# Optimization experiments

Hardware: AMD Instinct MI355X
Metric: run time of the kernel (lower is better)

Reference implementation:

```python
import jax, jax.numpy as jnp
import numpy as np

B, N, L, K, C1 = 128, 300, 600, 19, 100  # batch, num_cnns, input_length, filter_size, fc hidden
PS = 7  # pool size == stride
LC = L - (K - 1)               # 582, conv output length
LP = (LC - PS) // PS + 1       # 83, pooled length
NC = 2                         # num_classes
EPS = 1e-5


def _bn(x, g, b, m, v):
    # eval-mode batchnorm, params broadcast along given axes already
    return g * (x - m) * jax.lax.rsqrt(v + EPS) + b


def setup_inputs() -> dict:
    key = jax.random.key(0)
    ks = jax.random.split(key, 20)
    f = lambda i, shape, s=0.1: (jax.random.normal(ks[i], shape, dtype=jnp.float32) * s)
    pv = lambda i, shape: (jax.random.uniform(ks[i], shape, dtype=jnp.float32) + 0.5)
    return {
        'x': jax.random.normal(ks[0], (B, 4, L), dtype=jnp.float32),
        'conv_w': f(1, (N, 4, K)), 'conv_b': f(2, (N,)),
        'bn1_g': pv(3, (N,)), 'bn1_b': f(4, (N,)), 'bn1_m': f(5, (N,)), 'bn1_v': pv(6, (N,)),
        'fc1_w': f(7, (N, C1, LP)), 'fc1_b': f(8, (N, C1)),
        'bn2_g': pv(9, (N, C1)), 'bn2_b': f(10, (N, C1)), 'bn2_m': f(11, (N, C1)), 'bn2_v': pv(12, (N, C1)),
        'fc2_w': f(13, (N, C1)), 'fc2_b': f(14, (N,)),
        'bn3_g': pv(15, (N,)), 'bn3_b': f(16, (N,)), 'bn3_m': f(17, (N,)), 'bn3_v': pv(18, (N,)),
        'final_w': f(19, (NC, N)), 'final_b': jnp.zeros((NC,), dtype=jnp.float32),
    }


def reference(x, conv_w, conv_b, bn1_g, bn1_b, bn1_m, bn1_v,
              fc1_w, fc1_b, bn2_g, bn2_b, bn2_m, bn2_v,
              fc2_w, fc2_b, bn3_g, bn3_b, bn3_m, bn3_v,
              final_w, final_b):
    # grouped conv on a repeated input == plain conv with 4 in-channels, N out-channels
    h = jax.lax.conv_general_dilated(x, conv_w, window_strides=(1,), padding='VALID',
                                     dimension_numbers=('NCH', 'OIH', 'NCH'))  # [B,N,582]
    h = h + conv_b[None, :, None]
    h = _bn(h, bn1_g[None, :, None], bn1_b[None, :, None], bn1_m[None, :, None], bn1_v[None, :, None])
    h = jnp.exp(h)
    # MaxPool1d(7,7): [B,N,582] -> [B,N,83]
    h = jax.lax.reduce_window(h, -jnp.inf, jax.lax.max,
                              window_dimensions=(1, 1, PS), window_strides=(1, 1, PS), padding='VALID')
    # grouped 1x1 conv == per-unit dense: [B,N,83] x [N,100,83] -> [B,N,100]
    h = jnp.einsum('bnp,nhp->bnh', h, fc1_w) + fc1_b[None]
    h = jax.nn.relu(_bn(h, bn2_g[None], bn2_b[None], bn2_m[None], bn2_v[None]))
    # second grouped 1x1 conv: [B,N,100] x [N,100] -> [B,N]
    h = jnp.einsum('bnh,nh->bn', h, fc2_w) + fc2_b[None]
    h = jax.nn.relu(_bn(h, bn3_g[None], bn3_b[None], bn3_m[None], bn3_v[None]))
    return h @ final_w.T + final_b  # [B,num_classes]
```

## Files before the change

kernel.cpp:

```cpp
#include <hip/hip_runtime.h>
#include <math.h>

#define EPS_ 1e-5f

__global__ __launch_bounds__(256) void kP(const float* __restrict__ fc1w,
                                          const float* __restrict__ conv_w,
                                          float* __restrict__ w1T,
                                          float* __restrict__ cwT) {
    __shared__ float sm[22800];
    const int blk = blockIdx.x, tid = threadIdx.x;
    if (blk < 300) {
        for (int i = tid; i < 8300; i += 256) {
            const int h = i / 83, p = i - h * 83;
            sm[p * 101 + h] = fc1w[(size_t)blk * 8300 + i];
        }
        __syncthreads();
        for (int i = tid; i < 8300; i += 256) {
            const int p = i / 100, h = i - p * 100;
            w1T[(size_t)blk * 8300 + i] = sm[p * 101 + h];
        }
    } else {
        for (int i = tid; i < 22800; i += 256) sm[i] = conv_w[i];
        __syncthreads();
        for (int i = tid; i < 22800; i += 256) {
            const int k = i / 300, n = i - k * 300;
            cwT[i] = sm[n * 76 + k];
        }
    }
}

__global__ __launch_bounds__(64) void kA(
        const float* __restrict__ x,
        const float* __restrict__ cwT,
        const float* __restrict__ conv_b,
        const float* __restrict__ g1, const float* __restrict__ b1,
        const float* __restrict__ m1, const float* __restrict__ v1,
        float* __restrict__ pooled)
{
    const int id  = blockIdx.x;
    const int b   = id / 112;
    const int sub = id - b * 112;
    if (sub >= 105) return;
    const int ng  = sub / 21;
    const int pc  = sub - ng * 21;
    const int p0c = pc * 4;
    const int p0  = (p0c > 79) ? 79 : p0c;
    const int lane = threadIdx.x;
    const int n   = ng * 64 + lane;
    const int nc  = (n < 300) ? n : 299;

    float acc[28];
    #pragma unroll
    for (int i = 0; i < 28; ++i) acc[i] = 0.f;

    #pragma unroll 1
    for (int c = 0; c < 4; ++c) {
        const float* xc = x + b * 2400 + c * 600 + 7 * p0;
        float xw[46];
        #pragma unroll
        for (int j = 0; j < 46; ++j) xw[j] = xc[j];
        const float* wc = cwT + c * 19 * 300 + nc;
        #pragma unroll
        for (int k = 0; k < 19; ++k) {
            const float wv = wc[k * 300];
            #pragma unroll
            for (int p = 0; p < 4; ++p)
                #pragma unroll
                for (int q = 0; q < 7; ++q)
                    acc[p * 7 + q] = fmaf(xw[7 * p + q + k], wv, acc[p * 7 + q]);
        }
    }

    const float A1 = g1[nc] * rsqrtf(v1[nc] + EPS_);
    const float B1 = fmaf(A1, conv_b[nc] - m1[nc], b1[nc]);
    if (n < 300) {
        float* op = pooled + ((size_t)n * 83 + p0) * 128 + b;
        #pragma unroll
        for (int p = 0; p < 4; ++p) {
            float mx = -INFINITY;
            #pragma unroll
            for (int q = 0; q < 7; ++q)
                mx = fmaxf(mx, fmaf(A1, acc[p * 7 + q], B1));
            op[p * 128] = __expf(mx);
        }
    }
}

__global__ __launch_bounds__(128) void kB(
        const float* __restrict__ pooled,
        const float* __restrict__ w1T,
        const float* __restrict__ fc1b,
        const float* __restrict__ g2, const float* __restrict__ b2,
        const float* __restrict__ m2, const float* __restrict__ v2,
        const float* __restrict__ fc2w,
        const float* __restrict__ fc2b,
        const float* __restrict__ g3, const float* __restrict__ b3,
        const float* __restrict__ m3, const float* __restrict__ v3,
        float* __restrict__ sout)
{
    __shared__ float sRed[2][64];
    const int id = blockIdx.x;
    const int bh = id / 304;
    const int n  = id - bh * 304;
    if (n >= 300) return;
    const int tid  = threadIdx.x;
    const int lane = tid & 63;
    const int hh   = __builtin_amdgcn_readfirstlane(tid >> 6);
    const int h0   = hh * 50;
    const int bb   = bh * 64 + lane;

    const float* pp = pooled + (size_t)n * 83 * 128 + bb;
    const float* wp = w1T + (size_t)n * 8300 + h0;

    float acc[50];
    #pragma unroll
    for (int j = 0; j < 50; ++j) acc[j] = 0.f;

    #pragma unroll 2
    for (int p = 0; p < 83; ++p) {
        const float pv = pp[p * 128];
        #pragma unroll
        for (int j = 0; j < 50; ++j)
            acc[j] = fmaf(pv, wp[p * 100 + j], acc[j]);
    }

    const int base = n * 100 + h0;
    float part = 0.f;
    #pragma unroll
    for (int j = 0; j < 50; ++j) {
        const float A2 = g2[base + j] * rsqrtf(v2[base + j] + EPS_);
        const float C2 = fmaf(A2, fc1b[base + j] - m2[base + j], b2[base + j]);
        const float act = fmaxf(fmaf(A2, acc[j], C2), 0.f);
        part = fmaf(act, fc2w[base + j], part);
    }
    sRed[hh][lane] = part;
    __syncthreads();
    if (tid < 64) {
        float s = sRed[0][tid] + sRed[1][tid] + fc2b[n];
        const float A3 = g3[n] * rsqrtf(v3[n] + EPS_);
        const float z = fmaf(A3, s - m3[n], b3[n]);
        sout[n * 128 + bh * 64 + tid] = fmaxf(z, 0.f);
    }
}

__global__ __launch_bounds__(64) void kC(
        const float* __restrict__ sout,
        const float* __restrict__ fw,
        const float* __restrict__ fb,
        float* __restrict__ out)
{
    const int b = blockIdx.x, t = threadIdx.x;
    float a0 = 0.f, a1 = 0.f;
    for (int nn = t; nn < 300; nn += 64) {
        const float v = sout[nn * 128 + b];
        a0 = fmaf(v, fw[nn], a0);
        a1 = fmaf(v, fw[300 + nn], a1);
    }
    #pragma unroll
    for (int off = 32; off > 0; off >>= 1) {
        a0 += __shfl_xor(a0, off, 64);
        a1 += __shfl_xor(a1, off, 64);
    }
    if (t == 0) {
        out[b * 2 + 0] = a0 + fb[0];
        out[b * 2 + 1] = a1 + fb[1];
    }
}

extern "C" void kernel_launch(void* const* d_in, const int* in_sizes, int n_in,
                              void* d_out, int out_size, void* d_ws, size_t ws_size,
                              hipStream_t stream) {
    const float* x      = (const float*)d_in[0];
    const float* conv_w = (const float*)d_in[1];
    const float* conv_b = (const float*)d_in[2];
    const float* g1 = (const float*)d_in[3];
    const float* b1 = (const float*)d_in[4];
    const float* m1 = (const float*)d_in[5];
    const float* v1 = (const float*)d_in[6];
    const float* fc1_w = (const float*)d_in[7];
    const float* fc1_b = (const float*)d_in[8];
    const float* g2 = (const float*)d_in[9];
    const float* b2 = (const float*)d_in[10];
    const float* m2 = (const float*)d_in[11];
    const float* v2 = (const float*)d_in[12];
    const float* fc2_w = (const float*)d_in[13];
    const float* fc2_b = (const float*)d_in[14];
    const float* g3 = (const float*)d_in[15];
    const float* b3 = (const float*)d_in[16];
    const float* m3 = (const float*)d_in[17];
    const float* v3 = (const float*)d_in[18];
    const float* fw = (const float*)d_in[19];
    const float* fb = (const float*)d_in[20];
    float* out = (float*)d_out;

    float* pooled = (float*)d_ws;
    float* w1T    = pooled + (size_t)300 * 83 * 128;
    float* cwT    = w1T + (size_t)300 * 8300;
    float* sout   = cwT + 22800;

    kP<<<301, 256, 0, stream>>>(fc1_w, conv_w, w1T, cwT);
    kA<<<128 * 112, 64, 0, stream>>>(x, cwT, conv_b, g1, b1, m1, v1, pooled);
    kB<<<608, 128, 0, stream>>>(pooled, w1T, fc1_b, g2, b2, m2, v2,
                                fc2_w, fc2_b, g3, b3, m3, v3, sout);
    kC<<<128, 64, 0, stream>>>(sout, fw, fb, out);
}
```

Baseline: 189.8 us.

## Widen blocks across prep, conv and FC kernels to raise occupancy

The prep kernel no longer allocates a 91 KB shared array. Its conv-weight transpose is spread over 76 small blocks instead of one, which cuts LDS use and raises occupancy for the fc1 transpose blocks. The conv kernel packs four 64-lane work items into 256-thread blocks, giving fewer, larger blocks. The FC kernel splits the 100 hidden units over four waves (28/28/28/16) instead of two, which lowers register pressure per thread and adds parallelism. In exchange there is an uneven last wave and an extra shared-memory reduction step.

```diff
diff --git a/kernel.cpp b/kernel.cpp
--- a/kernel.cpp
+++ b/kernel.cpp
@@ -7,9 +7,9 @@
                                           const float* __restrict__ conv_w,
                                           float* __restrict__ w1T,
                                           float* __restrict__ cwT) {
-    __shared__ float sm[22800];
     const int blk = blockIdx.x, tid = threadIdx.x;
     if (blk < 300) {
+        __shared__ float sm[83 * 101];
         for (int i = tid; i < 8300; i += 256) {
             const int h = i / 83, p = i - h * 83;
             sm[p * 101 + h] = fc1w[(size_t)blk * 8300 + i];
@@ -20,16 +20,13 @@
             w1T[(size_t)blk * 8300 + i] = sm[p * 101 + h];
         }
     } else {
-        for (int i = tid; i < 22800; i += 256) sm[i] = conv_w[i];
-        __syncthreads();
-        for (int i = tid; i < 22800; i += 256) {
-            const int k = i / 300, n = i - k * 300;
-            cwT[i] = sm[n * 76 + k];
-        }
-    }
-}
-
-__global__ __launch_bounds__(64) void kA(
+        const int k = blk - 300;
+        for (int n = tid; n < 300; n += 256)
+            cwT[k * 300 + n] = conv_w[n * 76 + k];
+    }
+}
+
+__global__ __launch_bounds__(256) void kA(
         const float* __restrict__ x,
         const float* __restrict__ cwT,
         const float* __restrict__ conv_b,
@@ -38,14 +35,16 @@
         float* __restrict__ pooled)
 {
     const int id  = blockIdx.x;
-    const int b   = id / 112;
-    const int sub = id - b * 112;
+    const int b   = id >> 5;
+    const int g   = id & 31;
+    const int wv  = __builtin_amdgcn_readfirstlane(threadIdx.x >> 6);
+    const int sub = g * 4 + wv;
     if (sub >= 105) return;
     const int ng  = sub / 21;
     const int pc  = sub - ng * 21;
     const int p0c = pc * 4;
     const int p0  = (p0c > 79) ? 79 : p0c;
-    const int lane = threadIdx.x;
+    const int lane = threadIdx.x & 63;
     const int n   = ng * 64 + lane;
     const int nc  = (n < 300) ? n : 299;
 
@@ -62,12 +61,12 @@
         const float* wc = cwT + c * 19 * 300 + nc;
         #pragma unroll
         for (int k = 0; k < 19; ++k) {
-            const float wv = wc[k * 300];
+            const float wvv = wc[k * 300];
             #pragma unroll
             for (int p = 0; p < 4; ++p)
                 #pragma unroll
                 for (int q = 0; q < 7; ++q)
-                    acc[p * 7 + q] = fmaf(xw[7 * p + q + k], wv, acc[p * 7 + q]);
+                    acc[p * 7 + q] = fmaf(xw[7 * p + q + k], wvv, acc[p * 7 + q]);
         }
     }
 
@@ -86,7 +85,7 @@
     }
 }
 
-__global__ __launch_bounds__(128) void kB(
+__global__ __launch_bounds__(256) void kB(
         const float* __restrict__ pooled,
         const float* __restrict__ w1T,
         const float* __restrict__ fc1b,
@@ -98,45 +97,57 @@
         const float* __restrict__ m3, const float* __restrict__ v3,
         float* __restrict__ sout)
 {
-    __shared__ float sRed[2][64];
+    __shared__ float sRed[4][64];
     const int id = blockIdx.x;
     const int bh = id / 304;
     const int n  = id - bh * 304;
-    if (n >= 300) return;
     const int tid  = threadIdx.x;
     const int lane = tid & 63;
-    const int hh   = __builtin_amdgcn_readfirstlane(tid >> 6);
-    const int h0   = hh * 50;
+    const int wv   = __builtin_amdgcn_readfirstlane(tid >> 6);
+    const int h0   = wv * 28;
+    const int nh   = (wv < 3) ? 28 : 16;
     const int bb   = bh * 64 + lane;
 
-    const float* pp = pooled + (size_t)n * 83 * 128 + bb;
-    const float* wp = w1T + (size_t)n * 8300 + h0;
-
-    float acc[50];
-    #pragma unroll
-    for (int j = 0; j < 50; ++j) acc[j] = 0.f;
-
-    #pragma unroll 2
-    for (int p = 0; p < 83; ++p) {
-        const float pv = pp[p * 128];
-        #pragma unroll
-        for (int j = 0; j < 50; ++j)
-            acc[j] = fmaf(pv, wp[p * 100 + j], acc[j]);
-    }
-
-    const int base = n * 100 + h0;
     float part = 0.f;
-    #pragma unroll
-    for (int j = 0; j < 50; ++j) {
-        const float A2 = g2[base + j] * rsqrtf(v2[base + j] + EPS_);
-        const float C2 = fmaf(A2, fc1b[base + j] - m2[base + j], b2[base + j]);
-        const float act = fmaxf(fmaf(A2, acc[j], C2), 0.f);
-        part = fmaf(act, fc2w[base + j], part);
-    }
-    sRed[hh][lane] = part;
+    if (n < 300) {
+        const float* pp = pooled + (size_t)n * 83 * 128 + bb;
+        const float* wp = w1T + (size_t)n * 8300 + h0;
+
+        float acc[28];
+        #pragma unroll
+        for (int j = 0; j < 28; ++j) acc[j] = 0.f;
+
+        if (nh == 28) {
+            #pragma unroll 2
+            for (int p = 0; p < 83; ++p) {
+                const float pv = pp[p * 128];
+                #pragma unroll
+                for (int j = 0; j < 28; ++j)
+                    acc[j] = fmaf(pv, wp[p * 100 + j], acc[j]);
+            }
+        } else {
+            #pragma unroll 2
+            for (int p = 0; p < 83; ++p) {
+                const float pv = pp[p * 128];
+                #pragma unroll
+                for (int j = 0; j < 16; ++j)
+                    acc[j] = fmaf(pv, wp[p * 100 + j], acc[j]);
+            }
+        }
+
+        const int base = n * 100 + h0;
+        for (int j = 0; j < nh; ++j) {
+            const float A2 = g2[base + j] * rsqrtf(v2[base + j] + EPS_);
+            const float C2 = fmaf(A2, fc1b[base + j] - m2[base + j], b2[base + j]);
+            const float act = fmaxf(fmaf(A2, acc[j], C2), 0.f);
+            part = fmaf(act, fc2w[base + j], part);
+        }
+    }
+    sRed[wv][lane] = part;
     __syncthreads();
-    if (tid < 64) {
-        float s = sRed[0][tid] + sRed[1][tid] + fc2b[n];
+    if (tid < 64 && n < 300) {
+        float s = sRed[0][tid] + sRed[1][tid] + sRed[2][tid] + sRed[3][tid];
+        s += fc2b[n];
         const float A3 = g3[n] * rsqrtf(v3[n] + EPS_);
         const float z = fmaf(A3, s - m3[n], b3[n]);
         sout[n * 128 + bh * 64 + tid] = fmaxf(z, 0.f);
@@ -198,9 +209,9 @@
     float* cwT    = w1T + (size_t)300 * 8300;
     float* sout   = cwT + 22800;
 
-    kP<<<301, 256, 0, stream>>>(fc1_w, conv_w, w1T, cwT);
-    kA<<<128 * 112, 64, 0, stream>>>(x, cwT, conv_b, g1, b1, m1, v1, pooled);
-    kB<<<608, 128, 0, stream>>>(pooled, w1T, fc1_b, g2, b2, m2, v2,
+    kP<<<376, 256, 0, stream>>>(fc1_w, conv_w, w1T, cwT);
+    kA<<<128 * 32, 256, 0, stream>>>(x, cwT, conv_b, g1, b1, m1, v1, pooled);
+    kB<<<608, 256, 0, stream>>>(pooled, w1T, fc1_b, g2, b2, m2, v2,
                                 fc2_w, fc2_b, g3, b3, m3, v3, sout);
     kC<<<128, 64, 0, stream>>>(sout, fw, fb, out);
 }
```

Result: slower. 194.1 us (+2.3%).
